# Kernel optimization log

Measured on AMD Instinct MI355X. Metric: run time of the kernel, lower is better.

The kernel has to match this reference:

```python
import jax, jax.numpy as jnp
import numpy as np

HID = 64; N_LAYERS = 4; N_HEADS = 4; HEAD_DIM = 16; INTER = 32; MAXP = 1024; EPS = 1e-12


def setup_inputs() -> dict:
    key = jax.random.key(0)
    ks = iter(jax.random.split(key, 32))
    rn = lambda shape, s=0.02: jax.random.normal(next(ks), shape, jnp.float32) * s
    B, L = 32, 1024
    return {
        "features": jax.random.normal(next(ks), (B, L, HID), jnp.float32),
        "Wq": rn((N_LAYERS, HID, HID)), "bq": jnp.zeros((N_LAYERS, HID), jnp.float32),
        "Wk": rn((N_LAYERS, HID, HID)), "bk": jnp.zeros((N_LAYERS, HID), jnp.float32),
        "Wv": rn((N_LAYERS, HID, HID)), "bv": jnp.zeros((N_LAYERS, HID), jnp.float32),
        "Wo": rn((N_LAYERS, HID, HID)), "bo": jnp.zeros((N_LAYERS, HID), jnp.float32),
        "ln1_g": jnp.ones((N_LAYERS, HID), jnp.float32), "ln1_b": jnp.zeros((N_LAYERS, HID), jnp.float32),
        "Wi": rn((N_LAYERS, HID, INTER)), "bi": jnp.zeros((N_LAYERS, INTER), jnp.float32),
        "Wd": rn((N_LAYERS, INTER, HID)), "bd": jnp.zeros((N_LAYERS, HID), jnp.float32),
        "ln2_g": jnp.ones((N_LAYERS, HID), jnp.float32), "ln2_b": jnp.zeros((N_LAYERS, HID), jnp.float32),
        "rel_emb": rn((N_LAYERS, 2 * MAXP - 1, HEAD_DIM)),
        "fc_w": rn((HID, 6)), "fc_b": jnp.zeros((6,), jnp.float32),
    }


def _ln(x, g, b):
    m = jnp.mean(x, axis=-1, keepdims=True)
    v = jnp.mean((x - m) ** 2, axis=-1, keepdims=True)
    return (x - m) / jnp.sqrt(v + EPS) * g + b


def reference(features, Wq, bq, Wk, bk, Wv, bv, Wo, bo, ln1_g, ln1_b,
              Wi, bi, Wd, bd, ln2_g, ln2_b, rel_emb, fc_w, fc_b):
    B, L, _ = features.shape
    pos = jnp.arange(L)
    dist_idx = pos[:, None] - pos[None, :] + (MAXP - 1)  # [L, L] in [0, 2*MAXP-2]
    scale = np.float32(1.0 / np.sqrt(HEAD_DIM))

    def heads(t):  # [B,L,HID] -> [B,H,L,D]
        return t.reshape(B, L, N_HEADS, HEAD_DIM).transpose(0, 2, 1, 3)

    x = features
    for i in range(N_LAYERS):
        q = heads(x @ Wq[i] + bq[i])
        k = heads(x @ Wk[i] + bk[i])
        v = heads(x @ Wv[i] + bv[i])
        scores = jnp.einsum("bhld,bhrd->bhlr", q, k)
        pe = rel_emb[i][dist_idx]  # [L, L, D] relative_key positional embedding
        scores = scores + jnp.einsum("bhld,lrd->bhlr", q, pe)
        probs = jax.nn.softmax(scores * scale, axis=-1)
        ctx = jnp.einsum("bhlr,bhrd->bhld", probs, v).transpose(0, 2, 1, 3).reshape(B, L, HID)
        x = _ln(ctx @ Wo[i] + bo[i] + x, ln1_g[i], ln1_b[i])
        inter = jax.nn.gelu(x @ Wi[i] + bi[i], approximate=False)
        x = _ln(inter @ Wd[i] + bd[i] + x, ln2_g[i], ln2_b[i])
    return (x @ fc_w + fc_b)[:, 1:, :]
```

## Files before the change

kernel.cpp:

```cpp
#include <hip/hip_runtime.h>
#include <math.h>

static constexpr int Bc = 32;
static constexpr int Lc = 1024;

typedef _Float16 f16x4 __attribute__((ext_vector_type(4)));
typedef __fp16   h16x2 __attribute__((ext_vector_type(2)));
typedef float    f32x4 __attribute__((ext_vector_type(4)));

#define MFMA16(a, b, c) __builtin_amdgcn_mfma_f32_16x16x16f16((a), (b), (c), 0, 0, 0)

#if __has_builtin(__builtin_amdgcn_exp2f)
#define EXP2(x) __builtin_amdgcn_exp2f(x)
#else
#define EXP2(x) exp2f(x)
#endif

__global__ __launch_bounds__(256) void prep_kernel(
    const float* __restrict__ features, const float* __restrict__ rel,
    const float* __restrict__ Wq, const float* __restrict__ Wk,
    const float* __restrict__ Wv, const float* __restrict__ Wo,
    const float* __restrict__ Wi, const float* __restrict__ Wd,
    _Float16* __restrict__ xh, _Float16* __restrict__ relh,
    _Float16* __restrict__ wt)
{
    int i = blockIdx.x * 256 + threadIdx.x;
    {
        float4 v = ((const float4*)features)[i];
        h16x2 a = __builtin_amdgcn_cvt_pkrtz(v.x, v.y);
        h16x2 b = __builtin_amdgcn_cvt_pkrtz(v.z, v.w);
        f16x4 o; o[0] = a[0]; o[1] = a[1]; o[2] = b[0]; o[3] = b[1];
        ((f16x4*)xh)[i] = o;
    }
    if (i < 32752) {
        float4 v = ((const float4*)rel)[i];
        h16x2 a = __builtin_amdgcn_cvt_pkrtz(v.x, v.y);
        h16x2 b = __builtin_amdgcn_cvt_pkrtz(v.z, v.w);
        f16x4 o; o[0] = a[0]; o[1] = a[1]; o[2] = b[0]; o[3] = b[1];
        ((f16x4*)relh)[i] = o;
    }
    if (i < 65536) {
        int which = i >> 14, r = i & 16383;
        int m = r >> 12, k = (r >> 6) & 63, c = r & 63;
        const float* src = which == 0 ? Wq : which == 1 ? Wk : which == 2 ? Wv : Wo;
        wt[which * 16384 + m * 4096 + c * 64 + k] = (_Float16)src[r];
    } else if (i < 73728) {
        int r = i - 65536;
        int m = r >> 11, k = (r >> 5) & 63, c = r & 31;
        wt[65536 + m * 2048 + c * 64 + k] = (_Float16)Wi[r];
    } else if (i < 81920) {
        int r = i - 73728;
        int m = r >> 11, k = (r >> 6) & 31, c = r & 63;
        wt[73728 + m * 2048 + c * 32 + k] = (_Float16)Wd[r];
    }
}

__global__ __launch_bounds__(256) void qkv_kernel(
    const _Float16* __restrict__ xh,
    const _Float16* __restrict__ qT, const _Float16* __restrict__ kT,
    const _Float16* __restrict__ vT,
    const float* __restrict__ bq, const float* __restrict__ bk,
    const float* __restrict__ bv,
    _Float16* __restrict__ qo, _Float16* __restrict__ ko, _Float16* __restrict__ vt)
{
    const int t = threadIdx.x, wv = t >> 6, lane = t & 63, lo = lane & 15, hi = lane >> 4;
    const int row0 = blockIdx.x * 64 + wv * 16;
    const int b = row0 >> 10, l0 = row0 & 1023;

    f16x4 a[4];
    #pragma unroll
    for (int kk = 0; kk < 4; kk++)
        a[kk] = *(const f16x4*)(xh + (row0 + lo) * 64 + kk * 16 + 4 * hi);

    #pragma unroll
    for (int m = 0; m < 3; m++) {
        const _Float16* WT = m == 0 ? qT : m == 1 ? kT : vT;
        const float* bias  = m == 0 ? bq : m == 1 ? bk : bv;
        #pragma unroll
        for (int h = 0; h < 4; h++) {
            float bb = bias[h * 16 + lo];
            f32x4 acc = { bb, bb, bb, bb };
            #pragma unroll
            for (int kk = 0; kk < 4; kk++) {
                f16x4 bf = *(const f16x4*)(WT + (h * 16 + lo) * 64 + kk * 16 + 4 * hi);
                acc = MFMA16(a[kk], bf, acc);
            }
            int bh = b * 4 + h;
            if (m < 2) {
                _Float16* dst = (m == 0 ? qo : ko) + (bh * Lc + l0 + 4 * hi) * 16 + lo;
                dst[0]  = (_Float16)acc[0];
                dst[16] = (_Float16)acc[1];
                dst[32] = (_Float16)acc[2];
                dst[48] = (_Float16)acc[3];
            } else {
                h16x2 p0 = __builtin_amdgcn_cvt_pkrtz(acc[0], acc[1]);
                h16x2 p1 = __builtin_amdgcn_cvt_pkrtz(acc[2], acc[3]);
                f16x4 o; o[0] = p0[0]; o[1] = p0[1]; o[2] = p1[0]; o[3] = p1[1];
                *(f16x4*)(vt + (bh * 16 + lo) * Lc + l0 + 4 * hi) = o;
            }
        }
    }
}

__global__ __launch_bounds__(128) void attn_kernel(
    const _Float16* __restrict__ qg, const _Float16* __restrict__ kg,
    const _Float16* __restrict__ vtg, const _Float16* __restrict__ relh,
    _Float16* __restrict__ ctxh)
{
    __shared__ float Tl[2][2][16 * 68];
    const int wv = threadIdx.x >> 6, lane = threadIdx.x & 63;
    const int bh = blockIdx.x >> 4;
    const int l0 = (blockIdx.x & 15) * 64 + wv * 32;
    const int lo = lane & 15, hi = lane >> 4;
    float* ringA = Tl[wv][0];
    float* ringB = Tl[wv][1];

    const _Float16 qscale = (_Float16)0.36067376022224085f;
    f16x4 qfA = *(const f16x4*)(qg + (bh * Lc + l0 + lo) * 16 + 4 * hi);
    f16x4 qfB = *(const f16x4*)(qg + (bh * Lc + l0 + 16 + lo) * 16 + 4 * hi);
    #pragma unroll
    for (int j = 0; j < 4; j++) { qfA[j] *= qscale; qfB[j] *= qscale; }

    const int o = 12 + lo - 4 * hi;

    float* wrA0 = ringA + lo * 68 + 0  + 4 * hi;
    float* wrA1 = ringA + lo * 68 + 16 + 4 * hi;
    float* wrB0 = ringB + lo * 68 + 16 + 4 * hi;
    float* wrB1 = ringB + lo * 68 + 0  + 4 * hi;
    const float* rdA0 = ringA + lo * 68 + 0  + o;
    const float* rdA1 = ringA + lo * 68 + 16 + o;
    const float* rdB0 = ringB + lo * 68 + 16 + o;
    const float* rdB1 = ringB + lo * 68 + 0  + o;

    const _Float16* rbase = relh + 4 * hi;
    auto ldrel = [&](int row) {
        row = row > 2046 ? 2046 : row;
        return *(const f16x4*)(rbase + row * 16);
    };
    auto t_store = [&](f16x4 rf, f16x4 qf, float* wr) {
        f32x4 z = { 0.f, 0.f, 0.f, 0.f };
        f32x4 tt = MFMA16(rf, qf, z);
        *(f32x4*)(wr)      = tt;
        *(f32x4*)(wr + 32) = tt;
    };

    f16x4 P0 = ldrel(l0 + lo);
    f16x4 P1 = ldrel(l0 + 16 + lo);
    f16x4 P2 = ldrel(l0 + 32 + lo);
    t_store(P0, qfA, wrA0);
    t_store(P1, qfA, wrA1);
    t_store(P1, qfB, wrB0);
    t_store(P2, qfB, wrB1);

    f16x4 rfC = P2;
    int rrow = l0 + 48 + lo;
    f16x4 rfN = ldrel(rrow);
    rrow += 16;

    const _Float16* kp = kg  + (bh * Lc + 1008 + lo) * 16 + 4 * hi;
    const _Float16* vp = vtg + (bh * 16 + lo) * Lc + 1008 + 4 * hi;
    f16x4 kfc = *(const f16x4*)kp;
    f16x4 vfc = *(const f16x4*)vp;

    f32x4 otA = { 0.f, 0.f, 0.f, 0.f }, otB = { 0.f, 0.f, 0.f, 0.f };
    f32x4 dA  = { 0.f, 0.f, 0.f, 0.f }, dB  = { 0.f, 0.f, 0.f, 0.f };

    #pragma unroll 2
    for (int t = 0; t < 64; ++t) {
        kp -= 256; vp -= 16;
        f16x4 kfn = *(const f16x4*)kp;
        f16x4 vfn = *(const f16x4*)vp;
        f16x4 rf2 = ldrel(rrow); rrow += 16;

        const float* rdA = (t & 1) ? rdA1 : rdA0;
        const float* rdB = (t & 1) ? rdB1 : rdB0;
        f32x4 siA, siB;
        siA[0] = rdA[3]; siA[1] = rdA[2]; siA[2] = rdA[1]; siA[3] = rdA[0];
        siB[0] = rdB[3]; siB[1] = rdB[2]; siB[2] = rdB[1]; siB[3] = rdB[0];

        f32x4 sA = MFMA16(kfc, qfA, siA);
        f32x4 sB = MFMA16(kfc, qfB, siB);

        float eA0 = EXP2(sA[0]), eA1 = EXP2(sA[1]), eA2 = EXP2(sA[2]), eA3 = EXP2(sA[3]);
        float eB0 = EXP2(sB[0]), eB1 = EXP2(sB[1]), eB2 = EXP2(sB[2]), eB3 = EXP2(sB[3]);
        dA[0] += eA0; dA[1] += eA1; dA[2] += eA2; dA[3] += eA3;
        dB[0] += eB0; dB[1] += eB1; dB[2] += eB2; dB[3] += eB3;

        t_store(rfC, qfA, (t & 1) ? wrA1 : wrA0);
        t_store(rfN, qfB, (t & 1) ? wrB1 : wrB0);

        h16x2 pa = __builtin_amdgcn_cvt_pkrtz(eA0, eA1);
        h16x2 pb = __builtin_amdgcn_cvt_pkrtz(eA2, eA3);
        f16x4 pfA; pfA[0] = pa[0]; pfA[1] = pa[1]; pfA[2] = pb[0]; pfA[3] = pb[1];
        h16x2 pc = __builtin_amdgcn_cvt_pkrtz(eB0, eB1);
        h16x2 pd = __builtin_amdgcn_cvt_pkrtz(eB2, eB3);
        f16x4 pfB; pfB[0] = pc[0]; pfB[1] = pc[1]; pfB[2] = pd[0]; pfB[3] = pd[1];

        otA = MFMA16(vfc, pfA, otA);
        otB = MFMA16(vfc, pfB, otB);

        kfc = kfn; vfc = vfn;
        rfC = rfN; rfN = rf2;
    }

    const int b = bh >> 2, h = bh & 3;
    {
        float den = (dA[0] + dA[1]) + (dA[2] + dA[3]);
        den += __shfl_xor(den, 16);
        den += __shfl_xor(den, 32);
        const float inv = 1.f / den;
        h16x2 o0 = __builtin_amdgcn_cvt_pkrtz(otA[0] * inv, otA[1] * inv);
        h16x2 o1 = __builtin_amdgcn_cvt_pkrtz(otA[2] * inv, otA[3] * inv);
        f16x4 o4; o4[0] = o0[0]; o4[1] = o0[1]; o4[2] = o1[0]; o4[3] = o1[1];
        *(f16x4*)(ctxh + (b * Lc + l0 + lo) * 64 + h * 16 + 4 * hi) = o4;
    }
    {
        float den = (dB[0] + dB[1]) + (dB[2] + dB[3]);
        den += __shfl_xor(den, 16);
        den += __shfl_xor(den, 32);
        const float inv = 1.f / den;
        h16x2 o0 = __builtin_amdgcn_cvt_pkrtz(otB[0] * inv, otB[1] * inv);
        h16x2 o1 = __builtin_amdgcn_cvt_pkrtz(otB[2] * inv, otB[3] * inv);
        f16x4 o4; o4[0] = o0[0]; o4[1] = o0[1]; o4[2] = o1[0]; o4[3] = o1[1];
        *(f16x4*)(ctxh + (b * Lc + l0 + 16 + lo) * 64 + h * 16 + 4 * hi) = o4;
    }
}

__global__ __launch_bounds__(256) void tail_kernel(
    const _Float16* __restrict__ ctxh, const float* __restrict__ resid,
    const _Float16* __restrict__ woT, const float* __restrict__ bo,
    const float* __restrict__ g1, const float* __restrict__ b1,
    const _Float16* __restrict__ wiT, const float* __restrict__ bi,
    const _Float16* __restrict__ wdT, const float* __restrict__ bd,
    const float* __restrict__ g2, const float* __restrict__ b2,
    float* __restrict__ xout,
    int doq,
    const _Float16* __restrict__ qT, const _Float16* __restrict__ kT,
    const _Float16* __restrict__ vT,
    const float* __restrict__ bq, const float* __restrict__ bk,
    const float* __restrict__ bv,
    _Float16* __restrict__ qo, _Float16* __restrict__ ko, _Float16* __restrict__ vt)
{
    __shared__ _Float16 x1s[4][16 * 68];
    __shared__ _Float16 ins[4][16 * 36];
    const int t = threadIdx.x, wv = t >> 6, lane = t & 63, lo = lane & 15, hi = lane >> 4;
    const int row0 = blockIdx.x * 64 + wv * 16;

    f16x4 a[4];
    #pragma unroll
    for (int kk = 0; kk < 4; kk++)
        a[kk] = *(const f16x4*)(ctxh + (row0 + lo) * 64 + kk * 16 + 4 * hi);

    float c1[4][4];
    #pragma unroll
    for (int w = 0; w < 4; w++) {
        float bb = bo[w * 16 + lo];
        f32x4 acc;
        #pragma unroll
        for (int j = 0; j < 4; j++)
            acc[j] = bb + resid[(row0 + 4 * hi + j) * 64 + w * 16 + lo];
        #pragma unroll
        for (int kk = 0; kk < 4; kk++) {
            f16x4 bf = *(const f16x4*)(woT + (w * 16 + lo) * 64 + kk * 16 + 4 * hi);
            acc = MFMA16(a[kk], bf, acc);
        }
        #pragma unroll
        for (int j = 0; j < 4; j++) c1[w][j] = acc[j];
    }

    float x1[4][4];
    {
        float gg[4], bb2[4];
        #pragma unroll
        for (int w = 0; w < 4; w++) { gg[w] = g1[w * 16 + lo]; bb2[w] = b1[w * 16 + lo]; }
        #pragma unroll
        for (int j = 0; j < 4; j++) {
            float s = c1[0][j] + c1[1][j] + c1[2][j] + c1[3][j];
            float q = c1[0][j]*c1[0][j] + c1[1][j]*c1[1][j] + c1[2][j]*c1[2][j] + c1[3][j]*c1[3][j];
            #pragma unroll
            for (int off = 1; off < 16; off <<= 1) { s += __shfl_xor(s, off); q += __shfl_xor(q, off); }
            float m  = s * (1.f / 64.f);
            float vr = q * (1.f / 64.f) - m * m;
            float rs = rsqrtf(vr + 1e-12f);
            #pragma unroll
            for (int w = 0; w < 4; w++) x1[w][j] = (c1[w][j] - m) * rs * gg[w] + bb2[w];
        }
    }

    _Float16* xsp = x1s[wv];
    #pragma unroll
    for (int w = 0; w < 4; w++)
        #pragma unroll
        for (int j = 0; j < 4; j++)
            xsp[(4 * hi + j) * 68 + w * 16 + lo] = (_Float16)x1[w][j];
    f16x4 a2[4];
    #pragma unroll
    for (int kk = 0; kk < 4; kk++)
        a2[kk] = *(const f16x4*)(xsp + lo * 68 + kk * 16 + 4 * hi);

    float it[2][4];
    #pragma unroll
    for (int w = 0; w < 2; w++) {
        float bb = bi[w * 16 + lo];
        f32x4 acc = { bb, bb, bb, bb };
        #pragma unroll
        for (int kk = 0; kk < 4; kk++) {
            f16x4 bf = *(const f16x4*)(wiT + (w * 16 + lo) * 64 + kk * 16 + 4 * hi);
            acc = MFMA16(a2[kk], bf, acc);
        }
        #pragma unroll
        for (int j = 0; j < 4; j++) {
            float v = acc[j];
            it[w][j] = 0.5f * v * (1.f + erff(v * 0.70710678118654752f));
        }
    }

    _Float16* isp = ins[wv];
    #pragma unroll
    for (int w = 0; w < 2; w++)
        #pragma unroll
        for (int j = 0; j < 4; j++)
            isp[(4 * hi + j) * 36 + w * 16 + lo] = (_Float16)it[w][j];
    f16x4 a3[2];
    #pragma unroll
    for (int kk = 0; kk < 2; kk++)
        a3[kk] = *(const f16x4*)(isp + lo * 36 + kk * 16 + 4 * hi);

    float c2[4][4];
    #pragma unroll
    for (int w = 0; w < 4; w++) {
        float bb = bd[w * 16 + lo];
        f32x4 acc;
        #pragma unroll
        for (int j = 0; j < 4; j++) acc[j] = bb + x1[w][j];
        #pragma unroll
        for (int kk = 0; kk < 2; kk++) {
            f16x4 bf = *(const f16x4*)(wdT + (w * 16 + lo) * 32 + kk * 16 + 4 * hi);
            acc = MFMA16(a3[kk], bf, acc);
        }
        #pragma unroll
        for (int j = 0; j < 4; j++) c2[w][j] = acc[j];
    }

    float x2[4][4];
    {
        float gg[4], bb2[4];
        #pragma unroll
        for (int w = 0; w < 4; w++) { gg[w] = g2[w * 16 + lo]; bb2[w] = b2[w * 16 + lo]; }
        #pragma unroll
        for (int j = 0; j < 4; j++) {
            float s = c2[0][j] + c2[1][j] + c2[2][j] + c2[3][j];
            float q = c2[0][j]*c2[0][j] + c2[1][j]*c2[1][j] + c2[2][j]*c2[2][j] + c2[3][j]*c2[3][j];
            #pragma unroll
            for (int off = 1; off < 16; off <<= 1) { s += __shfl_xor(s, off); q += __shfl_xor(q, off); }
            float m  = s * (1.f / 64.f);
            float vr = q * (1.f / 64.f) - m * m;
            float rs = rsqrtf(vr + 1e-12f);
            #pragma unroll
            for (int w = 0; w < 4; w++) {
                float xv = (c2[w][j] - m) * rs * gg[w] + bb2[w];
                x2[w][j] = xv;
                xout[(row0 + 4 * hi + j) * 64 + w * 16 + lo] = xv;
            }
        }
    }

    if (!doq) return;

    #pragma unroll
    for (int w = 0; w < 4; w++)
        #pragma unroll
        for (int j = 0; j < 4; j++)
            xsp[(4 * hi + j) * 68 + w * 16 + lo] = (_Float16)x2[w][j];
    f16x4 aq[4];
    #pragma unroll
    for (int kk = 0; kk < 4; kk++)
        aq[kk] = *(const f16x4*)(xsp + lo * 68 + kk * 16 + 4 * hi);

    const int b = row0 >> 10, l0q = row0 & 1023;
    #pragma unroll
    for (int m = 0; m < 3; m++) {
        const _Float16* WT = m == 0 ? qT : m == 1 ? kT : vT;
        const float* bias  = m == 0 ? bq : m == 1 ? bk : bv;
        #pragma unroll
        for (int h = 0; h < 4; h++) {
            float bb = bias[h * 16 + lo];
            f32x4 acc = { bb, bb, bb, bb };
            #pragma unroll
            for (int kk = 0; kk < 4; kk++) {
                f16x4 bf = *(const f16x4*)(WT + (h * 16 + lo) * 64 + kk * 16 + 4 * hi);
                acc = MFMA16(aq[kk], bf, acc);
            }
            int bh = b * 4 + h;
            if (m < 2) {
                _Float16* dst = (m == 0 ? qo : ko) + (bh * Lc + l0q + 4 * hi) * 16 + lo;
                dst[0]  = (_Float16)acc[0];
                dst[16] = (_Float16)acc[1];
                dst[32] = (_Float16)acc[2];
                dst[48] = (_Float16)acc[3];
            } else {
                h16x2 p0 = __builtin_amdgcn_cvt_pkrtz(acc[0], acc[1]);
                h16x2 p1 = __builtin_amdgcn_cvt_pkrtz(acc[2], acc[3]);
                f16x4 o; o[0] = p0[0]; o[1] = p0[1]; o[2] = p1[0]; o[3] = p1[1];
                *(f16x4*)(vt + (bh * 16 + lo) * Lc + l0q + 4 * hi) = o;
            }
        }
    }
}

__global__ __launch_bounds__(256) void final_kernel(
    const float* __restrict__ x, const float* __restrict__ fcw,
    const float* __restrict__ fcb, float* __restrict__ out)
{
    int idx = blockIdx.x * 256 + threadIdx.x;
    if (idx >= Bc * 1023 * 6) return;
    int j = idx % 6;
    int rest = idx / 6;
    int l = rest % 1023 + 1;
    int b = rest / 1023;
    const float* xr = x + (b * Lc + l) * 64;
    float acc = fcb[j];
    for (int k = 0; k < 64; ++k) acc += xr[k] * fcw[k * 6 + j];
    out[idx] = acc;
}

extern "C" void kernel_launch(void* const* d_in, const int* in_sizes, int n_in,
                              void* d_out, int out_size, void* d_ws, size_t ws_size,
                              hipStream_t stream)
{
    (void)in_sizes; (void)n_in; (void)out_size; (void)ws_size;
    const float* features = (const float*)d_in[0];
    const float* Wq  = (const float*)d_in[1];
    const float* bq  = (const float*)d_in[2];
    const float* Wk  = (const float*)d_in[3];
    const float* bk  = (const float*)d_in[4];
    const float* Wv  = (const float*)d_in[5];
    const float* bv  = (const float*)d_in[6];
    const float* Wo  = (const float*)d_in[7];
    const float* bo  = (const float*)d_in[8];
    const float* g1  = (const float*)d_in[9];
    const float* b1  = (const float*)d_in[10];
    const float* Wi  = (const float*)d_in[11];
    const float* bi  = (const float*)d_in[12];
    const float* Wd  = (const float*)d_in[13];
    const float* bd  = (const float*)d_in[14];
    const float* g2  = (const float*)d_in[15];
    const float* b2  = (const float*)d_in[16];
    const float* rel = (const float*)d_in[17];
    const float* fcw = (const float*)d_in[18];
    const float* fcb = (const float*)d_in[19];
    float* out = (float*)d_out;

    char* ws = (char*)d_ws;
    float*    xbuf = (float*)(ws);
    _Float16* xh   = (_Float16*)(ws + ( 8u << 20));
    _Float16* ctxh = (_Float16*)(ws + (12u << 20));
    _Float16* qh   = (_Float16*)(ws + (16u << 20));
    _Float16* kh   = (_Float16*)(ws + (20u << 20));
    _Float16* vt   = (_Float16*)(ws + (24u << 20));
    _Float16* relh = (_Float16*)(ws + (28u << 20));
    _Float16* wt   = (_Float16*)(ws + (28u << 20) + (512u << 10));

    prep_kernel<<<2048, 256, 0, stream>>>(features, rel, Wq, Wk, Wv, Wo, Wi, Wd,
                                          xh, relh, wt);
    qkv_kernel<<<512, 256, 0, stream>>>(xh,
        wt, wt + 16384, wt + 32768, bq, bk, bv, qh, kh, vt);

    for (int i = 0; i < 4; ++i) {
        const float* resid = (i == 0) ? features : xbuf;
        int ni = i + 1;
        attn_kernel<<<2048, 128, 0, stream>>>(qh, kh, vt,
            relh + i * 2047 * 16, ctxh);
        tail_kernel<<<512, 256, 0, stream>>>(ctxh, resid,
            wt + 49152 + i * 4096, bo + i * 64, g1 + i * 64, b1 + i * 64,
            wt + 65536 + i * 2048, bi + i * 32,
            wt + 73728 + i * 2048, bd + i * 64, g2 + i * 64, b2 + i * 64,
            xbuf,
            (i < 3) ? 1 : 0,
            wt + ni * 4096, wt + 16384 + ni * 4096, wt + 32768 + ni * 4096,
            bq + ni * 64, bk + ni * 64, bv + ni * 64,
            qh, kh, vt);
    }
    final_kernel<<<768, 256, 0, stream>>>(xbuf, fcw, fcb, out);
}
```

Measured before the change: 315.6 us.

## Split attention key range across two waves with LDS reduction of partial outputs

Each block now handles 32 query rows instead of 64. Its two waves each process half of the 1024 keys, so the grid doubles to 4096 blocks. The partial numerators and denominators from wave 1 are combined with wave 0's through LDS after a __syncthreads, and wave 0 writes the output. The shared ring is shrunk and the mirrored T-stores are made conditional to cut LDS writes. The aim is more parallelism and shorter per-wave serial loops, at the cost of an extra barrier, an LDS reduction and an idle wave during the epilogue.

After: 329.6 us. +4.4%, slower.

```diff
diff --git a/kernel.cpp b/kernel.cpp
--- a/kernel.cpp
+++ b/kernel.cpp
@@ -107,10 +107,10 @@
     const _Float16* __restrict__ vtg, const _Float16* __restrict__ relh,
     _Float16* __restrict__ ctxh)
 {
-    __shared__ float Tl[2][2][16 * 68];
+    __shared__ float Tl[2][2][16 * 52];
     const int wv = threadIdx.x >> 6, lane = threadIdx.x & 63;
-    const int bh = blockIdx.x >> 4;
-    const int l0 = (blockIdx.x & 15) * 64 + wv * 32;
+    const int bh = blockIdx.x >> 5;
+    const int l0 = (blockIdx.x & 31) * 32;
     const int lo = lane & 15, hi = lane >> 4;
     float* ringA = Tl[wv][0];
     float* ringB = Tl[wv][1];
@@ -122,43 +122,45 @@
     for (int j = 0; j < 4; j++) { qfA[j] *= qscale; qfB[j] *= qscale; }
 
     const int o = 12 + lo - 4 * hi;
-
-    float* wrA0 = ringA + lo * 68 + 0  + 4 * hi;
-    float* wrA1 = ringA + lo * 68 + 16 + 4 * hi;
-    float* wrB0 = ringB + lo * 68 + 16 + 4 * hi;
-    float* wrB1 = ringB + lo * 68 + 0  + 4 * hi;
-    const float* rdA0 = ringA + lo * 68 + 0  + o;
-    const float* rdA1 = ringA + lo * 68 + 16 + o;
-    const float* rdB0 = ringB + lo * 68 + 16 + o;
-    const float* rdB1 = ringB + lo * 68 + 0  + o;
+    const int jb0 = l0 + 512 * wv;
+    const int rstart = 1008 - 512 * wv;
+
+    float* wrA_e = ringA + lo * 52 + 0  + 4 * hi;
+    float* wrA_o = ringA + lo * 52 + 16 + 4 * hi;
+    float* wrB_e = ringB + lo * 52 + 16 + 4 * hi;
+    float* wrB_o = ringB + lo * 52 + 0  + 4 * hi;
+    const float* rdA_e = ringA + lo * 52 + 0  + o;
+    const float* rdA_o = ringA + lo * 52 + 16 + o;
+    const float* rdB_e = ringB + lo * 52 + 16 + o;
+    const float* rdB_o = ringB + lo * 52 + 0  + o;
 
     const _Float16* rbase = relh + 4 * hi;
     auto ldrel = [&](int row) {
         row = row > 2046 ? 2046 : row;
         return *(const f16x4*)(rbase + row * 16);
     };
-    auto t_store = [&](f16x4 rf, f16x4 qf, float* wr) {
+    auto t_store = [&](f16x4 rf, f16x4 qf, float* wr, bool mir) {
         f32x4 z = { 0.f, 0.f, 0.f, 0.f };
         f32x4 tt = MFMA16(rf, qf, z);
-        *(f32x4*)(wr)      = tt;
-        *(f32x4*)(wr + 32) = tt;
+        *(f32x4*)(wr) = tt;
+        if (mir) *(f32x4*)(wr + 32) = tt;
     };
 
-    f16x4 P0 = ldrel(l0 + lo);
-    f16x4 P1 = ldrel(l0 + 16 + lo);
-    f16x4 P2 = ldrel(l0 + 32 + lo);
-    t_store(P0, qfA, wrA0);
-    t_store(P1, qfA, wrA1);
-    t_store(P1, qfB, wrB0);
-    t_store(P2, qfB, wrB1);
+    f16x4 P0 = ldrel(jb0 + lo);
+    f16x4 P1 = ldrel(jb0 + 16 + lo);
+    f16x4 P2 = ldrel(jb0 + 32 + lo);
+    t_store(P0, qfA, wrA_e, true);
+    t_store(P1, qfA, wrA_o, false);
+    t_store(P1, qfB, wrB_e, false);
+    t_store(P2, qfB, wrB_o, true);
 
     f16x4 rfC = P2;
-    int rrow = l0 + 48 + lo;
+    int rrow = jb0 + 48 + lo;
     f16x4 rfN = ldrel(rrow);
     rrow += 16;
 
-    const _Float16* kp = kg  + (bh * Lc + 1008 + lo) * 16 + 4 * hi;
-    const _Float16* vp = vtg + (bh * 16 + lo) * Lc + 1008 + 4 * hi;
+    const _Float16* kp = kg  + (bh * Lc + rstart + lo) * 16 + 4 * hi;
+    const _Float16* vp = vtg + (bh * 16 + lo) * Lc + rstart + 4 * hi;
     f16x4 kfc = *(const f16x4*)kp;
     f16x4 vfc = *(const f16x4*)vp;
 
@@ -166,14 +168,14 @@
     f32x4 dA  = { 0.f, 0.f, 0.f, 0.f }, dB  = { 0.f, 0.f, 0.f, 0.f };
 
     #pragma unroll 2
-    for (int t = 0; t < 64; ++t) {
+    for (int t = 0; t < 32; ++t) {
         kp -= 256; vp -= 16;
         f16x4 kfn = *(const f16x4*)kp;
         f16x4 vfn = *(const f16x4*)vp;
         f16x4 rf2 = ldrel(rrow); rrow += 16;
 
-        const float* rdA = (t & 1) ? rdA1 : rdA0;
-        const float* rdB = (t & 1) ? rdB1 : rdB0;
+        const float* rdA = (t & 1) ? rdA_o : rdA_e;
+        const float* rdB = (t & 1) ? rdB_o : rdB_e;
         f32x4 siA, siB;
         siA[0] = rdA[3]; siA[1] = rdA[2]; siA[2] = rdA[1]; siA[3] = rdA[0];
         siB[0] = rdB[3]; siB[1] = rdB[2]; siB[2] = rdB[1]; siB[3] = rdB[0];
@@ -186,8 +188,8 @@
         dA[0] += eA0; dA[1] += eA1; dA[2] += eA2; dA[3] += eA3;
         dB[0] += eB0; dB[1] += eB1; dB[2] += eB2; dB[3] += eB3;
 
-        t_store(rfC, qfA, (t & 1) ? wrA1 : wrA0);
-        t_store(rfN, qfB, (t & 1) ? wrB1 : wrB0);
+        t_store(rfC, qfA, (t & 1) ? wrA_o : wrA_e, !(t & 1));
+        t_store(rfN, qfB, (t & 1) ? wrB_o : wrB_e,  (t & 1));
 
         h16x2 pa = __builtin_amdgcn_cvt_pkrtz(eA0, eA1);
         h16x2 pb = __builtin_amdgcn_cvt_pkrtz(eA2, eA3);
@@ -203,26 +205,38 @@
         rfC = rfN; rfN = rf2;
     }
 
-    const int b = bh >> 2, h = bh & 3;
-    {
-        float den = (dA[0] + dA[1]) + (dA[2] + dA[3]);
-        den += __shfl_xor(den, 16);
-        den += __shfl_xor(den, 32);
-        const float inv = 1.f / den;
-        h16x2 o0 = __builtin_amdgcn_cvt_pkrtz(otA[0] * inv, otA[1] * inv);
-        h16x2 o1 = __builtin_amdgcn_cvt_pkrtz(otA[2] * inv, otA[3] * inv);
-        f16x4 o4; o4[0] = o0[0]; o4[1] = o0[1]; o4[2] = o1[0]; o4[3] = o1[1];
-        *(f16x4*)(ctxh + (b * Lc + l0 + lo) * 64 + h * 16 + 4 * hi) = o4;
-    }
-    {
-        float den = (dB[0] + dB[1]) + (dB[2] + dB[3]);
-        den += __shfl_xor(den, 16);
-        den += __shfl_xor(den, 32);
-        const float inv = 1.f / den;
-        h16x2 o0 = __builtin_amdgcn_cvt_pkrtz(otB[0] * inv, otB[1] * inv);
-        h16x2 o1 = __builtin_amdgcn_cvt_pkrtz(otB[2] * inv, otB[3] * inv);
-        f16x4 o4; o4[0] = o0[0]; o4[1] = o0[1]; o4[2] = o1[0]; o4[3] = o1[1];
-        *(f16x4*)(ctxh + (b * Lc + l0 + 16 + lo) * 64 + h * 16 + 4 * hi) = o4;
+    float* cb = &Tl[1][0][0];
+    if (wv == 1) {
+        *(f32x4*)(cb + lane * 12)     = otA;
+        *(f32x4*)(cb + lane * 12 + 4) = otB;
+        cb[lane * 12 + 8] = (dA[0] + dA[1]) + (dA[2] + dA[3]);
+        cb[lane * 12 + 9] = (dB[0] + dB[1]) + (dB[2] + dB[3]);
+    }
+    __syncthreads();
+    if (wv == 0) {
+        f32x4 pA = *(const f32x4*)(cb + lane * 12);
+        f32x4 pB = *(const f32x4*)(cb + lane * 12 + 4);
+        #pragma unroll
+        for (int j = 0; j < 4; j++) { otA[j] += pA[j]; otB[j] += pB[j]; }
+        float denA = (dA[0] + dA[1]) + (dA[2] + dA[3]) + cb[lane * 12 + 8];
+        float denB = (dB[0] + dB[1]) + (dB[2] + dB[3]) + cb[lane * 12 + 9];
+        denA += __shfl_xor(denA, 16); denA += __shfl_xor(denA, 32);
+        denB += __shfl_xor(denB, 16); denB += __shfl_xor(denB, 32);
+        const int b = bh >> 2, h = bh & 3;
+        {
+            const float inv = 1.f / denA;
+            h16x2 o0 = __builtin_amdgcn_cvt_pkrtz(otA[0] * inv, otA[1] * inv);
+            h16x2 o1 = __builtin_amdgcn_cvt_pkrtz(otA[2] * inv, otA[3] * inv);
+            f16x4 o4; o4[0] = o0[0]; o4[1] = o0[1]; o4[2] = o1[0]; o4[3] = o1[1];
+            *(f16x4*)(ctxh + (b * Lc + l0 + lo) * 64 + h * 16 + 4 * hi) = o4;
+        }
+        {
+            const float inv = 1.f / denB;
+            h16x2 o0 = __builtin_amdgcn_cvt_pkrtz(otB[0] * inv, otB[1] * inv);
+            h16x2 o1 = __builtin_amdgcn_cvt_pkrtz(otB[2] * inv, otB[3] * inv);
+            f16x4 o4; o4[0] = o0[0]; o4[1] = o0[1]; o4[2] = o1[0]; o4[3] = o1[1];
+            *(f16x4*)(ctxh + (b * Lc + l0 + 16 + lo) * 64 + h * 16 + 4 * hi) = o4;
+        }
     }
 }
 
@@ -469,7 +483,7 @@
     for (int i = 0; i < 4; ++i) {
         const float* resid = (i == 0) ? features : xbuf;
         int ni = i + 1;
-        attn_kernel<<<2048, 128, 0, stream>>>(qh, kh, vt,
+        attn_kernel<<<4096, 128, 0, stream>>>(qh, kh, vt,
             relh + i * 2047 * 16, ctxh);
         tail_kernel<<<512, 256, 0, stream>>>(ctxh, resid,
             wt + 49152 + i * 4096, bo + i * 64, g1 + i * 64, b1 + i * 64,
```
